# Kernel tuning notes

Measured on AMD Instinct MI355X. Metric: run time of the kernel, lower is better.

Reference implementation:

```python
import jax, jax.numpy as jnp
import numpy as np

ALPHA = 1.0
EPS = 1e-6

NUM_CLASSES = 100000
FEAT_DIM = 256
BATCH = 8192


def setup_inputs() -> dict:
    key = jax.random.key(0)
    k1, k2 = jax.random.split(key)
    features = jax.random.normal(k1, (BATCH, FEAT_DIM), dtype=jnp.float32)
    target = jax.random.randint(k2, (BATCH,), 0, NUM_CLASSES, dtype=jnp.int64)
    # centers bank initialized to zeros as in the torch module
    centers = jnp.zeros((NUM_CLASSES, FEAT_DIM), dtype=jnp.float32)
    return {"features": features, "target": target, "centers": centers}


def reference(features, target, centers):
    # gather per-sample class centers: [B, D]
    centers_batch = centers[target]
    # MSE loss over all elements (nn.MSELoss default reduction='mean')
    diff = centers_batch - features  # [B, D]
    center_loss = jnp.mean(diff * diff)
    # per-class appearance counts, gathered back per sample
    counts = jax.ops.segment_sum(
        jnp.ones((target.shape[0],), dtype=jnp.float32), target,
        num_segments=NUM_CLASSES)  # [C]
    appear = counts[target]  # [B]
    # per-sample scaled update, scatter-added into the centers bank
    upd = ALPHA * diff / (appear + EPS)[:, None]  # [B, D]
    delta = jax.ops.segment_sum(upd, target, num_segments=NUM_CLASSES)  # [C, D]
    new_centers = centers - delta
    return center_loss, new_centers
```

## Files before the change

### kernel.cpp

```cpp
#include <hip/hip_runtime.h>

#define BATCH   8192
#define FEAT    256
#define NCLASS  100000
#define EPS_C   1e-6f

#define NC_ELEMS (NCLASS * FEAT)
#define NVEC (NC_ELEMS / 4)
#define FUSED_BLOCKS (NVEC / 256)

__global__ void build_kernel(const int* __restrict__ target,
                             int* __restrict__ head,
                             int* __restrict__ next) {
    int b = blockIdx.x * blockDim.x + threadIdx.x;
    if (b < BATCH) next[b] = atomicExch(&head[target[b]], b);
}

__global__ void fused_kernel(const float* __restrict__ centers,
                             const float* __restrict__ features,
                             const int* __restrict__ head,
                             const int* __restrict__ next,
                             float* __restrict__ partials,
                             float* __restrict__ out ) {
    __shared__ float lds[1025];
    int w = threadIdx.x >> 6;
    int l = threadIdx.x & 63;
    int r = blockIdx.x * 4 + w;

    float4 c4 = ((const float4*)(centers + (size_t)r * FEAT))[l];
    float4 n4 = c4;
    int h = head[r];
    if (h != -1) {
        float4 sumf = {0.f, 0.f, 0.f, 0.f};
        int n = 0;
        for (int s = h; s != -1; s = next[s]) {
            float4 f4 = ((const float4*)(features + (size_t)s * FEAT))[l];
            sumf.x += f4.x; sumf.y += f4.y; sumf.z += f4.z; sumf.w += f4.w;
            float dx = c4.x - f4.x, dy = c4.y - f4.y;
            float dz = c4.z - f4.z, dw = c4.w - f4.w;
            float sq = dx*dx + dy*dy + dz*dz + dw*dw;
            #pragma unroll
            for (int off = 32; off > 0; off >>= 1) sq += __shfl_down(sq, off, 64);
            if (l == 0) partials[s] = sq;
            n++;
        }
        float nf = (float)n;
        float inv = 1.0f / (nf + EPS_C);
        n4.x = c4.x - (nf * c4.x - sumf.x) * inv;
        n4.y = c4.y - (nf * c4.y - sumf.y) * inv;
        n4.z = c4.z - (nf * c4.z - sumf.z) * inv;
        n4.w = c4.w - (nf * c4.w - sumf.w) * inv;
    }

    int base = 1 + w * 256 + 4 * l;
    lds[base + 0] = n4.x; lds[base + 1] = n4.y;
    lds[base + 2] = n4.z; lds[base + 3] = n4.w;

    if (threadIdx.x == 0) {
        float val = 0.0f;
        if (blockIdx.x > 0) {
            int rp = blockIdx.x * 4 - 1;
            float c = centers[(size_t)rp * FEAT + 255];
            val = c;
            int hp = head[rp];
            if (hp != -1) {
                float sf = 0.0f; int n = 0;
                for (int s = hp; s != -1; s = next[s]) {
                    sf += features[(size_t)s * FEAT + 255]; n++;
                }
                float nf = (float)n;
                val = c - (nf * c - sf) / (nf + EPS_C);
            }
        }
        lds[0] = val;
    }
    if (blockIdx.x == FUSED_BLOCKS - 1 && threadIdx.x == 255) {
        out[NC_ELEMS] = n4.w;
    }

    __syncthreads();

    int t = threadIdx.x;
    float4 ov;
    ov.x = lds[4*t + 0]; ov.y = lds[4*t + 1];
    ov.z = lds[4*t + 2]; ov.w = lds[4*t + 3];
    ((float4*)out)[(size_t)blockIdx.x * 256 + t] = ov;
}

__global__ void finalize_kernel(const float* __restrict__ partials,
                                float* __restrict__ out0) {
    float s = 0.0f;
    for (int i = threadIdx.x; i < BATCH; i += 256) s += partials[i];
    #pragma unroll
    for (int off = 32; off > 0; off >>= 1) s += __shfl_down(s, off, 64);
    __shared__ float red[4];
    int wave = threadIdx.x >> 6;
    int lane = threadIdx.x & 63;
    if (lane == 0) red[wave] = s;
    __syncthreads();
    if (threadIdx.x == 0) {
        out0[0] = (red[0] + red[1] + red[2] + red[3]) / (float)(BATCH * FEAT);
    }
}

extern "C" void kernel_launch(void* const* d_in, const int* in_sizes, int n_in,
                              void* d_out, int out_size, void* d_ws, size_t ws_size,
                              hipStream_t stream) {
    const float* features = (const float*)d_in[0];
    const int*   target   = (const int*)d_in[1];
    const float* centers  = (const float*)d_in[2];
    float* out = (float*)d_out;

    int*   head     = (int*)d_ws;
    int*   next     = head + NCLASS;
    float* partials = (float*)(next + BATCH);

    hipMemsetAsync(head, 0xFF, NCLASS * sizeof(int), stream);
    build_kernel<<<(BATCH + 255) / 256, 256, 0, stream>>>(target, head, next);
    fused_kernel<<<FUSED_BLOCKS, 256, 0, stream>>>(centers, features, head, next,
                                                   partials, out);
    finalize_kernel<<<1, 256, 0, stream>>>(partials, out);
}
```

Before: 196.6 us.

## Split fused kernel into dense shifted copy plus sparse per-class update

Replaces the single fused kernel, which checked the linked list for every one of 100k class rows, with two kernels. The first is a plain streaming copy of centers into the output at a one-float offset, using a wave shuffle and a small shared buffer to handle the shift. The second launches one wave per batch sample, keeps only the list-head wave for each class, and overwrites just the touched rows with updated values. This removes per-row head lookups and divergent list walks from the bandwidth-bound copy, at the cost of an extra launch and scattered unaligned row writes that must be ordered after the copy.

```diff
diff --git a/kernel.cpp b/kernel.cpp
--- a/kernel.cpp
+++ b/kernel.cpp
@@ -1,13 +1,13 @@
 #include <hip/hip_runtime.h>
 
-#define BATCH   8192
-#define FEAT    256
-#define NCLASS  100000
-#define EPS_C   1e-6f
+#define BATCH    8192
+#define FEAT     256
+#define NCLASS   100000
+#define EPS_C    1e-6f
 
 #define NC_ELEMS (NCLASS * FEAT)
-#define NVEC (NC_ELEMS / 4)
-#define FUSED_BLOCKS (NVEC / 256)
+#define NVEC     (NC_ELEMS / 4)
+#define COPY_BLOCKS (NVEC / 256)
 
 __global__ void build_kernel(const int* __restrict__ target,
                              int* __restrict__ head,
@@ -16,75 +16,68 @@
     if (b < BATCH) next[b] = atomicExch(&head[target[b]], b);
 }
 
-__global__ void fused_kernel(const float* __restrict__ centers,
-                             const float* __restrict__ features,
-                             const int* __restrict__ head,
-                             const int* __restrict__ next,
-                             float* __restrict__ partials,
-                             float* __restrict__ out ) {
-    __shared__ float lds[1025];
-    int w = threadIdx.x >> 6;
-    int l = threadIdx.x & 63;
-    int r = blockIdx.x * 4 + w;
+__global__ void copy_kernel(const float* __restrict__ centers,
+                            float* __restrict__ out) {
+    __shared__ float wtail[4];
+    int t = threadIdx.x;
+    int w = t >> 6;
+    int l = t & 63;
+    size_t i = (size_t)blockIdx.x * 256 + t;
+    float4 c4 = ((const float4*)centers)[i];
 
-    float4 c4 = ((const float4*)(centers + (size_t)r * FEAT))[l];
-    float4 n4 = c4;
-    int h = head[r];
-    if (h != -1) {
-        float4 sumf = {0.f, 0.f, 0.f, 0.f};
-        int n = 0;
-        for (int s = h; s != -1; s = next[s]) {
-            float4 f4 = ((const float4*)(features + (size_t)s * FEAT))[l];
-            sumf.x += f4.x; sumf.y += f4.y; sumf.z += f4.z; sumf.w += f4.w;
-            float dx = c4.x - f4.x, dy = c4.y - f4.y;
-            float dz = c4.z - f4.z, dw = c4.w - f4.w;
-            float sq = dx*dx + dy*dy + dz*dz + dw*dw;
-            #pragma unroll
-            for (int off = 32; off > 0; off >>= 1) sq += __shfl_down(sq, off, 64);
-            if (l == 0) partials[s] = sq;
-            n++;
+    float pw = __shfl_up(c4.w, 1, 64);
+    if (l == 63) wtail[w] = c4.w;
+    __syncthreads();
+    if (l == 0) {
+        if (w > 0) {
+            pw = wtail[w - 1];
+        } else if (blockIdx.x > 0) {
+            pw = centers[(size_t)blockIdx.x * 1024 - 1];
+        } else {
+            pw = 0.0f;
         }
-        float nf = (float)n;
-        float inv = 1.0f / (nf + EPS_C);
-        n4.x = c4.x - (nf * c4.x - sumf.x) * inv;
-        n4.y = c4.y - (nf * c4.y - sumf.y) * inv;
-        n4.z = c4.z - (nf * c4.z - sumf.z) * inv;
-        n4.w = c4.w - (nf * c4.w - sumf.w) * inv;
     }
+    float4 ov = {pw, c4.x, c4.y, c4.z};
+    ((float4*)out)[i] = ov;
 
-    int base = 1 + w * 256 + 4 * l;
-    lds[base + 0] = n4.x; lds[base + 1] = n4.y;
-    lds[base + 2] = n4.z; lds[base + 3] = n4.w;
+    if (blockIdx.x == COPY_BLOCKS - 1 && t == 255) out[NC_ELEMS] = c4.w;
+}
 
-    if (threadIdx.x == 0) {
-        float val = 0.0f;
-        if (blockIdx.x > 0) {
-            int rp = blockIdx.x * 4 - 1;
-            float c = centers[(size_t)rp * FEAT + 255];
-            val = c;
-            int hp = head[rp];
-            if (hp != -1) {
-                float sf = 0.0f; int n = 0;
-                for (int s = hp; s != -1; s = next[s]) {
-                    sf += features[(size_t)s * FEAT + 255]; n++;
-                }
-                float nf = (float)n;
-                val = c - (nf * c - sf) / (nf + EPS_C);
-            }
-        }
-        lds[0] = val;
+__global__ void update_kernel(const float* __restrict__ centers,
+                              const float* __restrict__ features,
+                              const int* __restrict__ target,
+                              const int* __restrict__ head,
+                              const int* __restrict__ next,
+                              float* __restrict__ partials,
+                              float* __restrict__ out) {
+    int wv = (blockIdx.x * blockDim.x + threadIdx.x) >> 6;
+    int l  = threadIdx.x & 63;
+    int r  = target[wv];
+    if (head[r] != wv) return;
+
+    const float4 c4 = ((const float4*)(centers + (size_t)r * FEAT))[l];
+    float4 sumf = {0.f, 0.f, 0.f, 0.f};
+    int n = 0;
+    for (int s = wv; s != -1; s = next[s]) {
+        float4 f4 = ((const float4*)(features + (size_t)s * FEAT))[l];
+        sumf.x += f4.x; sumf.y += f4.y; sumf.z += f4.z; sumf.w += f4.w;
+        float dx = c4.x - f4.x, dy = c4.y - f4.y;
+        float dz = c4.z - f4.z, dw = c4.w - f4.w;
+        float sq = dx*dx + dy*dy + dz*dz + dw*dw;
+        #pragma unroll
+        for (int off = 32; off > 0; off >>= 1) sq += __shfl_down(sq, off, 64);
+        if (l == 0) partials[s] = sq;
+        n++;
     }
-    if (blockIdx.x == FUSED_BLOCKS - 1 && threadIdx.x == 255) {
-        out[NC_ELEMS] = n4.w;
-    }
+    float nf  = (float)n;
+    float inv = 1.0f / (nf + EPS_C);
+    float nx = c4.x - (nf * c4.x - sumf.x) * inv;
+    float ny = c4.y - (nf * c4.y - sumf.y) * inv;
+    float nz = c4.z - (nf * c4.z - sumf.z) * inv;
+    float nw = c4.w - (nf * c4.w - sumf.w) * inv;
 
-    __syncthreads();
-
-    int t = threadIdx.x;
-    float4 ov;
-    ov.x = lds[4*t + 0]; ov.y = lds[4*t + 1];
-    ov.z = lds[4*t + 2]; ov.w = lds[4*t + 3];
-    ((float4*)out)[(size_t)blockIdx.x * 256 + t] = ov;
+    float* orow = out + 1 + (size_t)r * FEAT + 4 * l;
+    orow[0] = nx; orow[1] = ny; orow[2] = nz; orow[3] = nw;
 }
 
 __global__ void finalize_kernel(const float* __restrict__ partials,
@@ -117,7 +110,8 @@
 
     hipMemsetAsync(head, 0xFF, NCLASS * sizeof(int), stream);
     build_kernel<<<(BATCH + 255) / 256, 256, 0, stream>>>(target, head, next);
-    fused_kernel<<<FUSED_BLOCKS, 256, 0, stream>>>(centers, features, head, next,
-                                                   partials, out);
+    copy_kernel<<<COPY_BLOCKS, 256, 0, stream>>>(centers, out);
+    update_kernel<<<BATCH / 4, 256, 0, stream>>>(centers, features, target,
+                                                 head, next, partials, out);
     finalize_kernel<<<1, 256, 0, stream>>>(partials, out);
 }
```

New measurement: 205.7 us. 4.6% more time.
